# Kernel tuning notes

Measured on AMD Instinct MI355X. Metric: run time of the kernel, lower is better.

Reference implementation:

```python
import jax, jax.numpy as jnp
import numpy as np

BITS = 8
QMAX = float(2 ** (BITS - 1) - 1)  # 127 for 8-bit symmetric


def bits_quant(x):
    """8-bit symmetric per-tensor fake quantization (models the opaque bits_quant op)."""
    max_abs = jnp.max(jnp.abs(x))
    scale = jnp.where(max_abs > 0, max_abs / QMAX, 1.0).astype(x.dtype)
    q = jnp.clip(jnp.round(x / scale), -QMAX, QMAX) * scale
    return q


def quant_linear(x, w, b):
    # Q(Q(x @ w) + Q(b)) then Q of the result, per QuantLinearLayer.call
    y = bits_quant(jnp.matmul(x, w)) + bits_quant(b)
    return bits_quant(y)


def setup_inputs() -> dict:
    d = 4096
    key = jax.random.key(0)
    ks = jax.random.split(key, 12)
    s = 0.02
    return {
        "inputs": jax.random.normal(ks[0], (1, d), dtype=jnp.float32),
        "c": jax.random.normal(ks[1], (1, d), dtype=jnp.float32) * s,
        "h": jax.random.normal(ks[2], (1, d), dtype=jnp.float32) * s,
        "Wf_w": jax.random.normal(ks[3], (2 * d, d), dtype=jnp.float32) * s,
        "Wf_b": jax.random.normal(ks[4], (d,), dtype=jnp.float32) * s,
        "Wi_w": jax.random.normal(ks[5], (2 * d, d), dtype=jnp.float32) * s,
        "Wi_b": jax.random.normal(ks[6], (d,), dtype=jnp.float32) * s,
        "Wc_w": jax.random.normal(ks[7], (2 * d, d), dtype=jnp.float32) * s,
        "Wc_b": jax.random.normal(ks[8], (d,), dtype=jnp.float32) * s,
        "Wo_w": jax.random.normal(ks[9], (2 * d, d), dtype=jnp.float32) * s,
        "Wo_b": jax.random.normal(ks[10], (d,), dtype=jnp.float32) * s,
    }


def reference(inputs, c, h, Wf_w, Wf_b, Wi_w, Wi_b, Wc_w, Wc_b, Wo_w, Wo_b):
    # concat = Q([h, x])  -> [1, 2d]
    concat = bits_quant(jnp.concatenate([h, inputs], axis=1))
    z = bits_quant(jnp.tanh(quant_linear(concat, Wc_w, Wc_b)))
    zf = bits_quant(jax.nn.sigmoid(quant_linear(concat, Wf_w, Wf_b)))
    zi = bits_quant(jax.nn.sigmoid(quant_linear(concat, Wi_w, Wi_b)))
    zo = bits_quant(jax.nn.sigmoid(quant_linear(concat, Wo_w, Wo_b)))
    memory = bits_quant(z * zi)
    c_new = bits_quant(bits_quant(c * zf) + memory)
    h_new = bits_quant(zo * bits_quant(jnp.tanh(c_new)))
    return h_new
```

## Files before the change

kernel.cpp:

```cpp
#include <hip/hip_runtime.h>
#include <math.h>

#define QMAXF 127.0f

struct Ptrs4 { const float* p[4]; };

__device__ __forceinline__ float qscale(float m) {
    return (m > 0.0f) ? (m / QMAXF) : 1.0f;
}

__device__ __forceinline__ float quant1(float x, float s) {
    float r = rintf(x / s);
    r = fminf(fmaxf(r, -QMAXF), QMAXF);
    return r * s;
}

__device__ __forceinline__ float block_max_red(float v, float* sred) {
    #pragma unroll
    for (int off = 32; off > 0; off >>= 1)
        v = fmaxf(v, __shfl_down(v, off, 64));
    int wave = threadIdx.x >> 6;
    int lane = threadIdx.x & 63;
    __syncthreads();
    if (lane == 0) sred[wave] = v;
    __syncthreads();
    if (threadIdx.x == 0) {
        int nw = blockDim.x >> 6;
        float m = sred[0];
        for (int i = 1; i < nw; ++i) m = fmaxf(m, sred[i]);
        sred[16] = m;
    }
    __syncthreads();
    return sred[16];
}

__device__ __forceinline__ void quant_vec4(float* a, float* sred) {
    float pm = 0.0f;
    #pragma unroll
    for (int i = 0; i < 4; ++i) pm = fmaxf(pm, fabsf(a[i]));
    float s = qscale(block_max_red(pm, sred));
    #pragma unroll
    for (int i = 0; i < 4; ++i) a[i] = quant1(a[i], s);
}

__global__ __launch_bounds__(1024) void k_prep(
    const float* __restrict__ x, const float* __restrict__ h,
    Ptrs4 biases, float* __restrict__ concat_q, float* __restrict__ qb,
    unsigned* __restrict__ gmax)
{
    __shared__ float sred[17];
    int tid = threadIdx.x;
    if (blockIdx.x == 0) {
        if (tid < 4) gmax[tid] = 0u;
        float vals[8];
        float pm = 0.0f;
        #pragma unroll
        for (int i = 0; i < 8; ++i) {
            int idx = i * 1024 + tid;
            float v = (i < 4) ? h[idx] : x[idx - 4096];
            vals[i] = v;
            pm = fmaxf(pm, fabsf(v));
        }
        float s = qscale(block_max_red(pm, sred));
        #pragma unroll
        for (int i = 0; i < 8; ++i) concat_q[i * 1024 + tid] = quant1(vals[i], s);
    } else {
        int g = blockIdx.x - 1;
        const float* __restrict__ b = biases.p[g];
        float vals[4];
        float pm = 0.0f;
        #pragma unroll
        for (int i = 0; i < 4; ++i) {
            float v = b[i * 1024 + tid];
            vals[i] = v;
            pm = fmaxf(pm, fabsf(v));
        }
        float s = qscale(block_max_red(pm, sred));
        #pragma unroll
        for (int i = 0; i < 4; ++i) qb[g * 4096 + i * 1024 + tid] = quant1(vals[i], s);
    }
}

__global__ __launch_bounds__(256, 4) void k_gemv(
    Ptrs4 wts, const float* __restrict__ xq, float* __restrict__ partials)
{
    __shared__ float buf[2][8 * 512];

    int ct = blockIdx.x;
    int kc = blockIdx.y;
    int g  = blockIdx.z;
    const float* __restrict__ W = wts.p[g];
    int tid  = threadIdx.x;
    int wave = tid >> 6;
    int lane = tid & 63;
    int k0 = kc * 256;
    const float* __restrict__ wbase = W + (size_t)k0 * 4096 + ct * 512;
    const float* __restrict__ xp = xq + k0;

    auto stage = [&](const float* wsrc, float* lbuf) {
        #pragma unroll
        for (int j = 0; j < 4; ++j) {
            int t = wave * 4 + j;
            int row = t >> 1, half = t & 1;
            const float* src = wsrc + (size_t)row * 4096 + half * 256 + lane * 4;
            float* dst = lbuf + row * 512 + half * 256;
            __builtin_amdgcn_global_load_lds(
                (const __attribute__((address_space(1))) void*)src,
                (__attribute__((address_space(3))) void*)dst, 16, 0, 0);
        }
    };

    float ax = 0.f, ay = 0.f;

    stage(wbase, buf[0]);
    __syncthreads();
    int cur = 0;

    for (int kb = 0; kb < 256; kb += 8) {
        if (kb + 8 < 256)
            stage(wbase + (size_t)(kb + 8) * 4096, buf[cur ^ 1]);
        #pragma unroll
        for (int r = 0; r < 8; ++r) {
            float xv = xp[kb + r];
            float2 wv = *(const float2*)&buf[cur][r * 512 + tid * 2];
            ax = fmaf(xv, wv.x, ax);
            ay = fmaf(xv, wv.y, ay);
        }
        __syncthreads();
        cur ^= 1;
    }

    int col0 = ct * 512 + tid * 2;
    float2 r; r.x = ax; r.y = ay;
    *(float2*)(partials + (size_t)(g * 32 + kc) * 4096 + col0) = r;
}

__global__ __launch_bounds__(256) void k_reduce(
    const float* __restrict__ partials, float* __restrict__ y,
    unsigned* __restrict__ gmax)
{
    int g  = blockIdx.x >> 4;
    int cb = blockIdx.x & 15;
    int col = cb * 256 + threadIdx.x;
    float s = 0.0f;
    #pragma unroll 8
    for (int kc = 0; kc < 32; ++kc)
        s += partials[(size_t)(g * 32 + kc) * 4096 + col];
    y[g * 4096 + col] = s;

    float m = fabsf(s);
    #pragma unroll
    for (int off = 32; off > 0; off >>= 1)
        m = fmaxf(m, __shfl_down(m, off, 64));
    __shared__ float sm[4];
    int wave = threadIdx.x >> 6, lane = threadIdx.x & 63;
    if (lane == 0) sm[wave] = m;
    __syncthreads();
    if (threadIdx.x == 0) {
        float mm = fmaxf(fmaxf(sm[0], sm[1]), fmaxf(sm[2], sm[3]));
        atomicMax(gmax + g, __float_as_uint(mm));
    }
}

__global__ __launch_bounds__(1024) void k_epilogue(
    const float* __restrict__ y, const float* __restrict__ qb,
    const unsigned* __restrict__ gmax, const float* __restrict__ c,
    float* __restrict__ out)
{
    __shared__ float sred[17];
    int tid = threadIdx.x;
    float v[4][4];

    #pragma unroll
    for (int g = 0; g < 4; ++g) {
        float s = qscale(__uint_as_float(gmax[g]));
        #pragma unroll
        for (int i = 0; i < 4; ++i) {
            int col = i * 1024 + tid;
            v[g][i] = quant1(y[g * 4096 + col], s) + qb[g * 4096 + col];
        }
    }

    for (int g = 0; g < 4; ++g) {
        float pm = 0.0f;
        #pragma unroll
        for (int i = 0; i < 4; ++i) pm = fmaxf(pm, fabsf(v[g][i]));
        float s = qscale(block_max_red(pm, sred));
        #pragma unroll
        for (int i = 0; i < 4; ++i) {
            float q = quant1(v[g][i], s);
            v[g][i] = (g == 2) ? tanhf(q) : (1.0f / (1.0f + expf(-q)));
        }
    }

    for (int g = 0; g < 4; ++g) {
        float pm = 0.0f;
        #pragma unroll
        for (int i = 0; i < 4; ++i) pm = fmaxf(pm, fabsf(v[g][i]));
        float s = qscale(block_max_red(pm, sred));
        #pragma unroll
        for (int i = 0; i < 4; ++i) v[g][i] = quant1(v[g][i], s);
    }

    float mem[4];
    #pragma unroll
    for (int i = 0; i < 4; ++i) mem[i] = v[2][i] * v[1][i];
    quant_vec4(mem, sred);

    float cf[4];
    #pragma unroll
    for (int i = 0; i < 4; ++i) cf[i] = c[i * 1024 + tid] * v[0][i];
    quant_vec4(cf, sred);

    float cn[4];
    #pragma unroll
    for (int i = 0; i < 4; ++i) cn[i] = cf[i] + mem[i];
    quant_vec4(cn, sred);

    float tc[4];
    #pragma unroll
    for (int i = 0; i < 4; ++i) tc[i] = tanhf(cn[i]);
    quant_vec4(tc, sred);

    float hn[4];
    #pragma unroll
    for (int i = 0; i < 4; ++i) hn[i] = v[3][i] * tc[i];
    quant_vec4(hn, sred);
    #pragma unroll
    for (int i = 0; i < 4; ++i) out[i * 1024 + tid] = hn[i];
}

extern "C" void kernel_launch(void* const* d_in, const int* in_sizes, int n_in,
                              void* d_out, int out_size, void* d_ws, size_t ws_size,
                              hipStream_t stream) {
    const float* x = (const float*)d_in[0];
    const float* c = (const float*)d_in[1];
    const float* h = (const float*)d_in[2];
    Ptrs4 wts, bs;
    wts.p[0] = (const float*)d_in[3];  bs.p[0] = (const float*)d_in[4];
    wts.p[1] = (const float*)d_in[5];  bs.p[1] = (const float*)d_in[6];
    wts.p[2] = (const float*)d_in[7];  bs.p[2] = (const float*)d_in[8];
    wts.p[3] = (const float*)d_in[9];  bs.p[3] = (const float*)d_in[10];

    float* ws = (float*)d_ws;
    float* partials = ws;
    float* concat_q = ws + 524288;
    float* qb       = ws + 532480;
    float* yv       = ws + 548864;
    unsigned* gmax  = (unsigned*)(ws + 565248);

    hipLaunchKernelGGL(k_prep,     dim3(5),        dim3(1024), 0, stream,
                       x, h, bs, concat_q, qb, gmax);
    hipLaunchKernelGGL(k_gemv,     dim3(8, 32, 4), dim3(256),  0, stream,
                       wts, concat_q, partials);
    hipLaunchKernelGGL(k_reduce,   dim3(64),       dim3(256),  0, stream,
                       partials, yv, gmax);
    hipLaunchKernelGGL(k_epilogue, dim3(1),        dim3(1024), 0, stream,
                       yv, qb, gmax, c, (float*)d_out);
}
```

Measured before the change: 461.8 us.

## Deepen GEMV weight staging to a 4-slot LDS ring with explicit vmcnt waits

Replaces the double-buffered LDS staging in the GEMV with a 4-slot ring that keeps three stages of weight loads in flight. Each step waits with an explicit s_waitcnt vmcnt plus barrier instead of a full __syncthreads after every step. The x slice is also copied into shared memory once rather than read from global inside the loop. More bytes stay in flight per block, but LDS use grows to about 64KB per block and launch bounds drop to 2 blocks per SIMD, which may reduce occupancy.

```diff
diff --git a/kernel.cpp b/kernel.cpp
--- a/kernel.cpp
+++ b/kernel.cpp
@@ -81,10 +81,11 @@
     }
 }
 
-__global__ __launch_bounds__(256, 4) void k_gemv(
+__global__ __launch_bounds__(256, 2) void k_gemv(
     Ptrs4 wts, const float* __restrict__ xq, float* __restrict__ partials)
 {
-    __shared__ float buf[2][8 * 512];
+    __shared__ float ring[4][8 * 512];
+    __shared__ float x_s[256];
 
     int ct = blockIdx.x;
     int kc = blockIdx.y;
@@ -95,40 +96,52 @@
     int lane = tid & 63;
     int k0 = kc * 256;
     const float* __restrict__ wbase = W + (size_t)k0 * 4096 + ct * 512;
-    const float* __restrict__ xp = xq + k0;
-
-    auto stage = [&](const float* wsrc, float* lbuf) {
+
+    auto stage = [&](int st) {
+        const float* wsrc = wbase + (size_t)(st * 8) * 4096;
+        float* lbuf = &ring[st & 3][0];
         #pragma unroll
         for (int j = 0; j < 4; ++j) {
             int t = wave * 4 + j;
             int row = t >> 1, half = t & 1;
-            const float* src = wsrc + (size_t)row * 4096 + half * 256 + lane * 4;
-            float* dst = lbuf + row * 512 + half * 256;
             __builtin_amdgcn_global_load_lds(
-                (const __attribute__((address_space(1))) void*)src,
-                (__attribute__((address_space(3))) void*)dst, 16, 0, 0);
+                (const __attribute__((address_space(1))) void*)
+                    (wsrc + (size_t)row * 4096 + half * 256 + lane * 4),
+                (__attribute__((address_space(3))) void*)
+                    (lbuf + row * 512 + half * 256), 16, 0, 0);
         }
     };
 
     float ax = 0.f, ay = 0.f;
 
-    stage(wbase, buf[0]);
-    __syncthreads();
-    int cur = 0;
-
-    for (int kb = 0; kb < 256; kb += 8) {
-        if (kb + 8 < 256)
-            stage(wbase + (size_t)(kb + 8) * 4096, buf[cur ^ 1]);
+    auto compute = [&](int t) {
+        const float* sl = &ring[t & 3][0];
+        int kb = t * 8;
         #pragma unroll
         for (int r = 0; r < 8; ++r) {
-            float xv = xp[kb + r];
-            float2 wv = *(const float2*)&buf[cur][r * 512 + tid * 2];
+            float xv = x_s[kb + r];
+            float2 wv = *(const float2*)&sl[r * 512 + tid * 2];
             ax = fmaf(xv, wv.x, ax);
             ay = fmaf(xv, wv.y, ay);
         }
-        __syncthreads();
-        cur ^= 1;
-    }
+    };
+
+    #define WAITBAR(N) asm volatile("s_waitcnt vmcnt(" #N ") lgkmcnt(0)\ns_barrier" ::: "memory")
+
+    x_s[tid] = xq[k0 + tid];
+    __syncthreads();
+    stage(0); stage(1); stage(2);
+
+    for (int t = 0; t < 30; ++t) {
+        WAITBAR(8);
+        compute(t);
+        if (t + 3 < 32) stage(t + 3);
+    }
+    WAITBAR(4);
+    compute(30);
+    WAITBAR(0);
+    compute(31);
+    #undef WAITBAR
 
     int col0 = ct * 512 + tid * 2;
     float2 r; r.x = ax; r.y = ay;
```

After: 479.9 us. 1.04x slower.
